# Kernel tuning notes

Hardware: AMD Instinct MI355X
Metric: run time of the kernel (lower is better)

## Reference

```python
import jax, jax.numpy as jnp
import numpy as np

B, N, U, D = 64, 1024, 128, 2   # batch, num_nodes, num_units, output_dim
K, L = 2, 2                     # max_diffusion_step, num_layers
NM = 2 * K + 1                  # num_matrices: 2 supports (dual random walk) * K + identity


def setup_inputs():
    key = jax.random.key(0)
    ks = jax.random.split(key, 16)
    d0, d1 = D + U, U + U       # gconv input_size per layer
    s = 0.05
    return {
        "inputs": jax.random.normal(ks[0], (B, N * D), jnp.float32),
        "hidden_state": jax.random.normal(ks[1], (L, B, N * U), jnp.float32),
        "adj": jax.random.uniform(ks[2], (N, N), dtype=jnp.float32),
        "gate_w0": jax.random.normal(ks[3], (d0 * NM, 2 * U), jnp.float32) * s,
        "gate_b0": jnp.ones((2 * U,), jnp.float32),   # bias_start=1.0 as in DCGRU gate
        "cand_w0": jax.random.normal(ks[4], (d0 * NM, U), jnp.float32) * s,
        "cand_b0": jnp.zeros((U,), jnp.float32),
        "gate_w1": jax.random.normal(ks[5], (d1 * NM, 2 * U), jnp.float32) * s,
        "gate_b1": jnp.ones((2 * U,), jnp.float32),
        "cand_w1": jax.random.normal(ks[6], (d1 * NM, U), jnp.float32) * s,
        "cand_b1": jnp.zeros((U,), jnp.float32),
        "proj_w": jax.random.normal(ks[7], (U, D), jnp.float32) * s,
        "proj_b": jnp.zeros((D,), jnp.float32),
    }


def _supports(adj):
    # dual random walk: [ (D_o^-1 A)^T, (D_i^-1 A^T)^T ]
    rw = lambda a: a / jnp.sum(a, axis=1, keepdims=True)
    return [rw(adj).T, rw(adj.T).T]


def _gconv(supports, x_bnd, h_bnd, w, b):
    # x_bnd: (B,N,in_dim), h_bnd: (B,N,U)
    in_size = x_bnd.shape[-1] + U
    x0 = jnp.transpose(jnp.concatenate([x_bnd, h_bnd], axis=-1), (1, 2, 0)).reshape(N, in_size * B)
    xs = [x0]
    for S in supports:
        xk_2, xk_1 = x0, S @ x0
        xs.append(xk_1)
        for _ in range(2, K + 1):
            xk = 2.0 * (S @ xk_1) - xk_2   # Chebyshev recursion
            xs.append(xk)
            xk_2, xk_1 = xk_1, xk
    x = jnp.stack(xs)                                   # (NM, N, in_size*B)
    x = x.reshape(NM, N, in_size, B).transpose(3, 1, 2, 0).reshape(B * N, in_size * NM)
    return x @ w + b                                    # (B*N, out)


def _dcgru_cell(supports, x_flat, h_flat, gw, gb, cw, cb, in_dim):
    xb = x_flat.reshape(B, N, in_dim)
    hb = h_flat.reshape(B, N, U)
    ru = jax.nn.sigmoid(_gconv(supports, xb, hb, gw, gb)).reshape(B, N, 2 * U)
    r, u = ru[..., :U], ru[..., U:]
    c = jnp.tanh(_gconv(supports, xb, r * hb, cw, cb)).reshape(B, N, U)
    return (u * hb + (1.0 - u) * c).reshape(B, N * U)


def reference(inputs, hidden_state, adj, gate_w0, gate_b0, cand_w0, cand_b0,
              gate_w1, gate_b1, cand_w1, cand_b1, proj_w, proj_b):
    sup = _supports(adj)
    h0 = _dcgru_cell(sup, inputs, hidden_state[0], gate_w0, gate_b0, cand_w0, cand_b0, D)
    h1 = _dcgru_cell(sup, h0, hidden_state[1], gate_w1, gate_b1, cand_w1, cand_b1, U)
    out = (h1.reshape(B * N, U) @ proj_w + proj_b).reshape(B, N * D)
    return out, jnp.stack([h0, h1])
```

## Files before the change

kernel.cpp:

```cpp
#include <hip/hip_runtime.h>
#include <hip/hip_bf16.h>

typedef unsigned short u16;
typedef unsigned int u32;
typedef __attribute__((ext_vector_type(2))) unsigned int u32x2;
typedef __attribute__((ext_vector_type(4))) float f32x4;
typedef __attribute__((ext_vector_type(8))) __bf16 bf16x8;

#define DEVI static __device__ __forceinline__

DEVI u16 f2bf(float x) {
  union { float f; u32 u; } v; v.f = x;
  u32 r = v.u + 0x7fffu + ((v.u >> 16) & 1u);
  return (u16)(r >> 16);
}
DEVI float bf2f(u16 h) { union { u32 u; float f; } v; v.u = ((u32)h) << 16; return v.f; }
DEVI u32 pk2bf(float a, float b) { return (u32)f2bf(a) | ((u32)f2bf(b) << 16); }
DEVI float sigm(float x) { return 1.f / (1.f + __expf(-x)); }
DEVI float tanh_(float x) {
  float a = fabsf(x);
  float e = __expf(-2.f * a);
  float t = (1.f - e) / (1.f + e);
  return copysignf(t, x);
}

DEVI void gl_lds16(const u16* g, void* l) {
  __builtin_amdgcn_global_load_lds(
      (const __attribute__((address_space(1))) u32*)(const void*)g,
      (__attribute__((address_space(3))) u32*)l, 16, 0, 0);
}
DEVI f32x4 mfma16(bf16x8 a, bf16x8 b, f32x4 c) {
  return __builtin_amdgcn_mfma_f32_16x16x32_bf16(a, b, c, 0, 0, 0);
}

#define SWZ(row) (((row) >> 1) & 3)

__global__ void sums_k(const float* __restrict__ adj, float* __restrict__ rs, float* __restrict__ cs) {
  __shared__ float red[256];
  int bid = blockIdx.x, tid = threadIdx.x;
  if (bid < 1024) {
    float a = 0.f;
    for (int j = tid; j < 1024; j += 256) a += adj[bid * 1024 + j];
    red[tid] = a; __syncthreads();
    for (int s = 128; s; s >>= 1) { if (tid < s) red[tid] += red[tid + s]; __syncthreads(); }
    if (!tid) rs[bid] = red[0];
  } else {
    int c0 = (bid - 1024) * 64;
    int c = tid & 63, r0 = tid >> 6;
    float a = 0.f;
    for (int r = r0; r < 1024; r += 4) a += adj[r * 1024 + c0 + c];
    red[tid] = a; __syncthreads();
    if (tid < 64) cs[c0 + c] = red[c] + red[64 + c] + red[128 + c] + red[192 + c];
  }
}

__global__ void s0_build(const float* __restrict__ adj, const float* __restrict__ rs, u16* __restrict__ S0) {
  __shared__ float tile[32][33];
  int i0 = blockIdx.x * 32, j0 = blockIdx.y * 32;
  int tx = threadIdx.x & 31, ty = threadIdx.x >> 5;
  for (int yy = ty; yy < 32; yy += 8)
    tile[yy][tx] = adj[(j0 + yy) * 1024 + i0 + tx];
  __syncthreads();
  for (int yy = ty; yy < 32; yy += 8)
    S0[(i0 + yy) * 1024 + j0 + tx] = f2bf(tile[tx][yy] / rs[j0 + tx]);
}

__global__ void s1_build(const float* __restrict__ adj, const float* __restrict__ cs, u16* __restrict__ S1) {
  int idx = blockIdx.x * 256 + threadIdx.x;
  int j = idx & 1023;
  S1[idx] = f2bf(adj[idx] / cs[j]);
}

__global__ void pack_w(const float* __restrict__ src, u16* __restrict__ dst,
                       int NO, int Ktot, int off0, int off1) {
  int idx = blockIdx.x * 256 + threadIdx.x;
  if (idx >= NO * Ktot) return;
  int o = idx / Ktot, k = idx % Ktot;
  int seg = k >> 7, i = k & 127;
  int mo = seg % 5;
  int pos = ((seg / 5) ? off1 : off0) + i;
  const float* wr = src + (long)pos * 5 * NO + o;
  float v;
  switch (mo) {
    case 0: v = wr[0] - wr[(long)2 * NO] - wr[(long)4 * NO]; break;
    case 1: v = wr[(long)1 * NO]; break;
    case 2: v = 2.f * wr[(long)2 * NO]; break;
    case 3: v = wr[(long)3 * NO]; break;
    default: v = 2.f * wr[(long)4 * NO]; break;
  }
  dst[idx] = f2bf(v);
}

__global__ void build_hx(const float* __restrict__ src, u16* __restrict__ hiN,
                         u16* __restrict__ hiT) {
  __shared__ u16 t[32][33];
  int n0 = blockIdx.x * 32, u0 = blockIdx.y * 32, b = blockIdx.z;
  int tx = threadIdx.x & 31, ty = threadIdx.x >> 5;
  for (int yy = ty; yy < 32; yy += 8) {
    long d = (long)b * 131072 + (n0 + yy) * 128 + u0 + tx;
    u16 h = f2bf(src[d]);
    hiN[d] = h;
    t[yy][tx] = h;
  }
  __syncthreads();
  for (int yy = ty; yy < 32; yy += 8)
    hiT[(long)(b * 128 + u0 + yy) * 1024 + n0 + tx] = t[tx][yy];
}

__global__ void xch0_build(const float* __restrict__ inp, float* __restrict__ x0) {
  int idx = blockIdx.x * 256 + threadIdx.x;
  int n = idx >> 7, c = idx & 127, b = c >> 1, d = c & 1;
  x0[idx] = inp[b * 2048 + n * 2 + d];
}

struct XJob { const u16* S; const float* xin; const float* x0; float* xout; };
struct XJobs { XJob j[2]; };
__global__ void xch_step2(XJobs js) {
  XJob J = js.j[blockIdx.z];
  int n = blockIdx.x, c = threadIdx.x;
  float acc = 0.f;
  for (int k = 0; k < 1024; k++) acc += bf2f(J.S[n * 1024 + k]) * J.xin[k * 128 + c];
  J.xout[n * 128 + c] = (J.x0 != nullptr) ? (2.f * acc - J.x0[n * 128 + c]) : acc;
}

__global__ __launch_bounds__(256) void xg_build(
    const float* __restrict__ gw0, const float* __restrict__ cw0,
    const float* __restrict__ xch,
    u16* __restrict__ xgg, u16* __restrict__ xgc) {
  __shared__ float wg[10][256];
  __shared__ float wc[10][128];
  __shared__ float xv[10];
  int t = threadIdx.x;
#pragma unroll
  for (int q = 0; q < 10; q++) {
    int m = q % 5, p = q / 5;
    wg[q][t] = gw0[(long)(p * 5 + m) * 256 + t];
    if (t < 128) wc[q][t] = cw0[(long)(p * 5 + m) * 128 + t];
  }
  __syncthreads();
  int r0 = blockIdx.x * 32;
  for (int rl = 0; rl < 32; rl++) {
    int r = r0 + rl, n = r & 1023, b = r >> 10;
    if (t < 10) { int m = t % 5, p = t / 5; xv[t] = xch[(long)m * 131072 + n * 128 + b * 2 + p]; }
    __syncthreads();
    float a = 0.f;
#pragma unroll
    for (int q = 0; q < 10; q++) a += wg[q][t] * xv[q];
    xgg[(long)r * 256 + t] = f2bf(a);
    if (t < 128) {
      float a2 = 0.f;
#pragma unroll
      for (int q = 0; q < 10; q++) a2 += wc[q][t] * xv[q];
      xgc[(long)r * 128 + t] = f2bf(a2);
    }
    __syncthreads();
  }
}

struct DiffJob { const u16* X; const u16* S; u16* YN; u16* YT; };
struct DiffJobs { DiffJob j[4]; };

__global__ __launch_bounds__(256, 2) void gemm_diffz(DiffJobs jobs) {
  DiffJob J = jobs.j[blockIdx.z];
  constexpr int BUF = 384 * 64;
  __shared__ char smem[3 * BUF];
  const int tid = threadIdx.x, wid = tid >> 6, lane = tid & 63;
  const int wrM = wid >> 1, wcN = wid & 1, l15 = lane & 15, l4 = lane >> 4;
  const int s_row = lane >> 2, s_kcp = lane & 3;
  const int l = blockIdx.y * 64 + blockIdx.x;
  const int sl = (l & 7) * 32 + (l >> 3);
  const int fbase = (sl >> 2) * 128;
  const int ntile = (sl & 3) * 256;

  f32x4 acc[8][4];
#pragma unroll
  for (int i = 0; i < 8; i++)
#pragma unroll
    for (int j = 0; j < 4; j++) acc[i][j] = (f32x4){0.f, 0.f, 0.f, 0.f};

  auto stage = [&](char* buf, int ks) {
    const int k0 = ks * 32;
#pragma unroll
    for (int c = 0; c < 6; c++) {
      const int row0 = c * 64 + wid * 16;
      const int row = row0 + s_row;
      const u16* src;
      if (row0 < 256) src = J.S + (long)(ntile + row) * 1024 + k0 + ((s_kcp ^ SWZ(row)) * 8);
      else { const int fr = row - 256; src = J.X + (long)(fbase + fr) * 1024 + k0 + ((s_kcp ^ SWZ(fr)) * 8); }
      gl_lds16(src, buf + row0 * 64);
    }
  };
  auto compute = [&](char* buf) {
    char* Ab = buf; char* Bb = buf + 256 * 64;
    bf16x8 af[8], bfr[4];
#pragma unroll
    for (int mb = 0; mb < 8; mb++) {
      const int row = wrM * 128 + mb * 16 + l15;
      af[mb] = *(const bf16x8*)(Ab + row * 64 + ((l4 ^ SWZ(row)) * 16));
    }
#pragma unroll
    for (int nb = 0; nb < 4; nb++) {
      const int row = wcN * 64 + nb * 16 + l15;
      bfr[nb] = *(const bf16x8*)(Bb + row * 64 + ((l4 ^ SWZ(row)) * 16));
    }
    __builtin_amdgcn_s_setprio(1);
#pragma unroll
    for (int mb = 0; mb < 8; mb++)
#pragma unroll
      for (int nb = 0; nb < 4; nb++)
        acc[mb][nb] = mfma16(af[mb], bfr[nb], acc[mb][nb]);
    __builtin_amdgcn_s_setprio(0);
  };

  const int NKS = 32;
  stage(smem, 0);
  stage(smem + BUF, 1);
  char* cur = smem; char* mid = smem + BUF; char* fut = smem + 2 * BUF;
  for (int ks = 0; ks + 2 < NKS; ks++) {
    stage(fut, ks + 2);
    asm volatile("s_waitcnt vmcnt(12)" ::: "memory");
    __builtin_amdgcn_s_barrier();
    __builtin_amdgcn_sched_barrier(0);
    compute(cur);
    asm volatile("" ::: "memory");
    __builtin_amdgcn_s_barrier();
    __builtin_amdgcn_sched_barrier(0);
    char* t = cur; cur = mid; mid = fut; fut = t;
  }
  asm volatile("s_waitcnt vmcnt(6)" ::: "memory");
  __builtin_amdgcn_s_barrier();
  __builtin_amdgcn_sched_barrier(0);
  compute(cur);
  asm volatile("s_waitcnt vmcnt(0)" ::: "memory");
  __builtin_amdgcn_s_barrier();
  __builtin_amdgcn_sched_barrier(0);
  compute(mid);

#pragma unroll
  for (int mb = 0; mb < 8; mb++) {
#pragma unroll
    for (int nb = 0; nb < 4; nb++) {
      const int n0 = ntile + wrM * 128 + mb * 16 + l4 * 4;
      const int f  = fbase + wcN * 64 + nb * 16 + l15;
      const int b = f >> 7, u = f & 127;
      f32x4 v = acc[mb][nb];
      u16 h0 = f2bf(v[0]), h1 = f2bf(v[1]), h2 = f2bf(v[2]), h3 = f2bf(v[3]);
      u16* yn = J.YN + (long)b * 131072 + (long)n0 * 128 + u;
      yn[0] = h0; yn[128] = h1; yn[256] = h2; yn[384] = h3;
      if (J.YT != nullptr) {
        u32x2 wv; wv[0] = (u32)h0 | ((u32)h1 << 16); wv[1] = (u32)h2 | ((u32)h3 << 16);
        *(u32x2*)(J.YT + (long)f * 1024 + n0) = wv;
      }
    }
  }
}

struct Segs { const u16* p[10]; };
DEVI const u16* seg_sel(const Segs& s, int i) {
  switch (i) {
    case 0: return s.p[0]; case 1: return s.p[1]; case 2: return s.p[2];
    case 3: return s.p[3]; case 4: return s.p[4]; case 5: return s.p[5];
    case 6: return s.p[6]; case 7: return s.p[7]; case 8: return s.p[8];
    default: return s.p[9];
  }
}

template<int EPI>
__global__ __launch_bounds__(256, 2) void gemm_wseg(
    Segs segs, const u16* __restrict__ WT, int Ktot,
    const float* __restrict__ bias, const float* __restrict__ Hprev,
    const u16* __restrict__ Hb16,
    const u16* __restrict__ xadd,
    u16* __restrict__ rh_hi, u16* __restrict__ rh_t, u16* __restrict__ usig,
    float* __restrict__ hnew_out, u16* __restrict__ xa_hi, u16* __restrict__ xa_t)
{
  constexpr int TM = (EPI == 0) ? 256 : 128;
  constexpr int MB = (EPI == 0) ? 8 : 4;
  constexpr int MW = (EPI == 0) ? 128 : 64;
  constexpr int R1 = (TM + 128) / 64;
  constexpr int BUF = (TM + 128) * 64;
  __shared__ char smem[3 * BUF];
  const int tid = threadIdx.x, wid = tid >> 6, lane = tid & 63;
  const int wrM = wid >> 1, wcN = wid & 1, l15 = lane & 15, l4 = lane >> 4;
  const int s_row = lane >> 2, s_kcp = lane & 3;
  const int rtile = blockIdx.x * 128;

  f32x4 acc[MB][4];
#pragma unroll
  for (int i = 0; i < MB; i++)
#pragma unroll
    for (int j = 0; j < 4; j++) acc[i][j] = (f32x4){0.f, 0.f, 0.f, 0.f};

  const int NKS = Ktot >> 5;
  auto stage = [&](char* buf, int ks) {
    const int k0 = ks * 32;
    const int sidx = ks >> 2, si0 = (ks & 3) * 32;
    const u16* sp = seg_sel(segs, sidx);
#pragma unroll
    for (int c = 0; c < R1; c++) {
      const int row0 = c * 64 + wid * 16;
      const int row = row0 + s_row;
      const u16* src;
      if (row0 < TM) src = WT + (long)row * Ktot + k0 + ((s_kcp ^ SWZ(row)) * 8);
      else { const int br = row - TM; src = sp + (long)(rtile + br) * 128 + si0 + ((s_kcp ^ SWZ(br)) * 8); }
      gl_lds16(src, buf + row0 * 64);
    }
  };
  auto compute = [&](char* buf) {
    char* Ab = buf; char* Bb = buf + TM * 64;
    bf16x8 af[MB], bfr[4];
#pragma unroll
    for (int mb = 0; mb < MB; mb++) {
      const int row = wrM * MW + mb * 16 + l15;
      af[mb] = *(const bf16x8*)(Ab + row * 64 + ((l4 ^ SWZ(row)) * 16));
    }
#pragma unroll
    for (int nb = 0; nb < 4; nb++) {
      const int row = wcN * 64 + nb * 16 + l15;
      bfr[nb] = *(const bf16x8*)(Bb + row * 64 + ((l4 ^ SWZ(row)) * 16));
    }
    __builtin_amdgcn_s_setprio(1);
#pragma unroll
    for (int mb = 0; mb < MB; mb++)
#pragma unroll
      for (int nb = 0; nb < 4; nb++)
        acc[mb][nb] = mfma16(af[mb], bfr[nb], acc[mb][nb]);
    __builtin_amdgcn_s_setprio(0);
  };

  stage(smem, 0);
  stage(smem + BUF, 1);
  char* cur = smem; char* mid = smem + BUF; char* fut = smem + 2 * BUF;
  for (int ks = 0; ks + 2 < NKS; ks++) {
    stage(fut, ks + 2);
    if constexpr (R1 == 6) asm volatile("s_waitcnt vmcnt(12)" ::: "memory");
    else                   asm volatile("s_waitcnt vmcnt(8)" ::: "memory");
    __builtin_amdgcn_s_barrier();
    __builtin_amdgcn_sched_barrier(0);
    compute(cur);
    asm volatile("" ::: "memory");
    __builtin_amdgcn_s_barrier();
    __builtin_amdgcn_sched_barrier(0);
    char* t = cur; cur = mid; mid = fut; fut = t;
  }
  if constexpr (R1 == 6) asm volatile("s_waitcnt vmcnt(6)" ::: "memory");
  else                   asm volatile("s_waitcnt vmcnt(4)" ::: "memory");
  __builtin_amdgcn_s_barrier();
  __builtin_amdgcn_sched_barrier(0);
  compute(cur);
  asm volatile("s_waitcnt vmcnt(0)" ::: "memory");
  __builtin_amdgcn_s_barrier();
  __builtin_amdgcn_sched_barrier(0);
  compute(mid);

#pragma unroll
  for (int mb = 0; mb < MB; mb++) {
#pragma unroll
    for (int nb = 0; nb < 4; nb++) {
      const int o = wrM * MW + mb * 16 + l4 * 4;
      const int rr = rtile + wcN * 64 + nb * 16 + l15;
      const int n = rr & 1023, b = rr >> 10;
      f32x4 v = acc[mb][nb];
      float4 bv = *(const float4*)(bias + o);
      float a0 = 0.f, a1 = 0.f, a2 = 0.f, a3 = 0.f;
      if (xadd != nullptr) {
        const int xs = (EPI == 0) ? 256 : 128;
        u32x2 xv = *(const u32x2*)(xadd + (long)rr * xs + o);
        a0 = bf2f((u16)(xv[0] & 0xffffu)); a1 = bf2f((u16)(xv[0] >> 16));
        a2 = bf2f((u16)(xv[1] & 0xffffu)); a3 = bf2f((u16)(xv[1] >> 16));
      }
      float hx0, hx1, hx2, hx3;
      if (Hb16 != nullptr) {
        u32x2 hv2 = *(const u32x2*)(Hb16 + (long)rr * 128 + o);
        hx0 = bf2f((u16)(hv2[0] & 0xffffu)); hx1 = bf2f((u16)(hv2[0] >> 16));
        hx2 = bf2f((u16)(hv2[1] & 0xffffu)); hx3 = bf2f((u16)(hv2[1] >> 16));
      } else {
        float4 hv = *(const float4*)(Hprev + (long)rr * 128 + o);
        hx0 = hv.x; hx1 = hv.y; hx2 = hv.z; hx3 = hv.w;
      }
      if (EPI == 0) {
        float s0 = sigm(v[0] + bv.x + a0), s1 = sigm(v[1] + bv.y + a1);
        float s2 = sigm(v[2] + bv.z + a2), s3 = sigm(v[3] + bv.w + a3);
        if (o < 128) {
          float r0 = s0 * hx0, r1 = s1 * hx1, r2 = s2 * hx2, r3 = s3 * hx3;
          u16 h0 = f2bf(r0), h1 = f2bf(r1), h2 = f2bf(r2), h3 = f2bf(r3);
          long d = (long)rr * 128 + o;
          u32x2 wh; wh[0] = (u32)h0 | ((u32)h1 << 16); wh[1] = (u32)h2 | ((u32)h3 << 16);
          *(u32x2*)(rh_hi + d) = wh;
          u16* rt = rh_t + (long)(b * 128 + o) * 1024 + n;
          rt[0] = h0; rt[1024] = h1; rt[2048] = h2; rt[3072] = h3;
        } else {
          u32x2 wu; wu[0] = pk2bf(s0, s1); wu[1] = pk2bf(s2, s3);
          *(u32x2*)(usig + (long)rr * 128 + (o - 128)) = wu;
        }
      } else {
        float c0 = tanh_(v[0] + bv.x + a0), c1 = tanh_(v[1] + bv.y + a1);
        float c2 = tanh_(v[2] + bv.z + a2), c3 = tanh_(v[3] + bv.w + a3);
        u32x2 uv = *(const u32x2*)(usig + (long)rr * 128 + o);
        float u0 = bf2f((u16)(uv[0] & 0xffffu)), u1 = bf2f((u16)(uv[0] >> 16));
        float u2 = bf2f((u16)(uv[1] & 0xffffu)), u3 = bf2f((u16)(uv[1] >> 16));
        float h0n = u0 * hx0 + (1.f - u0) * c0;
        float h1n = u1 * hx1 + (1.f - u1) * c1;
        float h2n = u2 * hx2 + (1.f - u2) * c2;
        float h3n = u3 * hx3 + (1.f - u3) * c3;
        *(float4*)(hnew_out + (long)rr * 128 + o) = make_float4(h0n, h1n, h2n, h3n);
        if (xa_hi != nullptr) {
          u16 x0 = f2bf(h0n), x1 = f2bf(h1n), x2 = f2bf(h2n), x3 = f2bf(h3n);
          long d = (long)rr * 128 + o;
          u32x2 wh; wh[0] = (u32)x0 | ((u32)x1 << 16); wh[1] = (u32)x2 | ((u32)x3 << 16);
          *(u32x2*)(xa_hi + d) = wh;
          u16* xt = xa_t + (long)(b * 128 + o) * 1024 + n;
          xt[0] = x0; xt[1024] = x1; xt[2048] = x2; xt[3072] = x3;
        }
      }
    }
  }
}

__global__ __launch_bounds__(256) void proj_k(const float* __restrict__ h1n, const float* __restrict__ pw,
                                              const float* __restrict__ pb, float* __restrict__ out) {
  int wid = threadIdx.x >> 6, lane = threadIdx.x & 63;
  int r = blockIdx.x * 4 + wid;
  int b = r >> 10, n = r & 1023;
  const float* hp = h1n + (long)b * 131072 + n * 128;
  float ha = hp[lane], hb = hp[lane + 64];
  float p0 = ha * pw[lane * 2]     + hb * pw[(lane + 64) * 2];
  float p1 = ha * pw[lane * 2 + 1] + hb * pw[(lane + 64) * 2 + 1];
  for (int off = 32; off; off >>= 1) { p0 += __shfl_down(p0, off); p1 += __shfl_down(p1, off); }
  if (!lane) {
    out[(long)b * 2048 + n * 2]     = p0 + pb[0];
    out[(long)b * 2048 + n * 2 + 1] = p1 + pb[1];
  }
}

extern "C" void kernel_launch(void* const* d_in, const int* in_sizes, int n_in,
                              void* d_out, int out_size, void* d_ws, size_t ws_size,
                              hipStream_t stream) {
  (void)in_sizes; (void)n_in; (void)out_size; (void)ws_size;
  const float* inputs = (const float*)d_in[0];
  const float* hidden = (const float*)d_in[1];
  const float* adj    = (const float*)d_in[2];
  const float* gw0 = (const float*)d_in[3];
  const float* gb0 = (const float*)d_in[4];
  const float* cw0 = (const float*)d_in[5];
  const float* cb0 = (const float*)d_in[6];
  const float* gw1 = (const float*)d_in[7];
  const float* gb1 = (const float*)d_in[8];
  const float* cw1 = (const float*)d_in[9];
  const float* cb1 = (const float*)d_in[10];
  const float* pw  = (const float*)d_in[11];
  const float* pb  = (const float*)d_in[12];

  float* out    = (float*)d_out;
  float* out_h0 = out + 131072;
  float* out_h1 = out_h0 + 8388608;
  const float* h0 = hidden;
  const float* h1 = hidden + 8388608;

  u16* OH1a = (u16*)out_h1;

  char* wp = (char*)d_ws;
  auto alloc = [&](size_t bytes) { char* r = wp; wp += (bytes + 255) & ~(size_t)255; return r; };
  u16*   S0b  = (u16*)  alloc(1048576 * 2);
  u16*   S1b  = (u16*)  alloc(1048576 * 2);
  float* rs   = (float*)alloc(1024 * 4);
  float* cs   = (float*)alloc(1024 * 4);
  u16*   WG0  = (u16*)  alloc((size_t)256 * 640 * 2);
  u16*   WC0  = (u16*)  alloc((size_t)128 * 640 * 2);
  u16*   WG1  = (u16*)  alloc((size_t)256 * 1280 * 2);
  u16*   WC1  = (u16*)  alloc((size_t)128 * 1280 * 2);
  u16*   Bb   = (u16*)  alloc((size_t)13 * 8388608 * 2);
  u16*   USIG = (u16*)  alloc((size_t)8388608 * 2);
  float* XCH  = (float*)alloc((size_t)5 * 131072 * 4);
  auto BB = [&](int i) { return Bb + (size_t)i * 8388608; };
  auto XC = [&](int i) { return XCH + (size_t)i * 131072; };
  u16* XGg = BB(3);
  u16* XGc = BB(5);

  sums_k<<<1040, 256, 0, stream>>>(adj, rs, cs);
  s0_build<<<dim3(32, 32), 256, 0, stream>>>(adj, rs, S0b);
  s1_build<<<4096, 256, 0, stream>>>(adj, cs, S1b);
  pack_w<<<640,  256, 0, stream>>>(gw0, WG0, 256, 640, 2, 0);
  pack_w<<<320,  256, 0, stream>>>(cw0, WC0, 128, 640, 2, 0);
  pack_w<<<1280, 256, 0, stream>>>(gw1, WG1, 256, 1280, 0, 128);
  pack_w<<<640,  256, 0, stream>>>(cw1, WC1, 128, 1280, 0, 128);
  build_hx<<<dim3(32, 4, 64), 256, 0, stream>>>(h0, BB(0), BB(1));
  build_hx<<<dim3(32, 4, 64), 256, 0, stream>>>(h1, OH1a, BB(2));

  xch0_build<<<512, 256, 0, stream>>>(inputs, XC(0));
  XJobs xj{};
  xj.j[0] = {S0b, XC(0), nullptr, XC(1)};
  xj.j[1] = {S1b, XC(0), nullptr, XC(3)};
  xch_step2<<<dim3(1024, 1, 2), 128, 0, stream>>>(xj);
  xj.j[0] = {S0b, XC(1), XC(0), XC(2)};
  xj.j[1] = {S1b, XC(3), XC(0), XC(4)};
  xch_step2<<<dim3(1024, 1, 2), 128, 0, stream>>>(xj);
  xg_build<<<2048, 256, 0, stream>>>(gw0, cw0, XCH, XGg, XGc);

  DiffJobs dj{};
  dj.j[0] = {BB(1), S0b, BB(6), BB(7)};
  dj.j[1] = {BB(1), S1b, BB(8), BB(9)};
  gemm_diffz<<<dim3(64, 4, 2), 256, 0, stream>>>(dj);
  dj.j[0] = {BB(7), S0b, BB(10), nullptr};
  dj.j[1] = {BB(9), S1b, BB(11), nullptr};
  gemm_diffz<<<dim3(64, 4, 2), 256, 0, stream>>>(dj);

  Segs sg0{};
  sg0.p[0] = BB(0); sg0.p[1] = BB(6); sg0.p[2] = BB(10); sg0.p[3] = BB(8); sg0.p[4] = BB(11);
  gemm_wseg<0><<<512, 256, 0, stream>>>(sg0, WG0, 640, gb0, h0, BB(0), XGg,
      BB(12), BB(1), USIG, nullptr, nullptr, nullptr);

  dj.j[0] = {BB(1), S0b, BB(6), BB(7)};
  dj.j[1] = {BB(1), S1b, BB(8), BB(9)};
  gemm_diffz<<<dim3(64, 4, 2), 256, 0, stream>>>(dj);
  dj.j[0] = {BB(7), S0b, BB(10), nullptr};
  dj.j[1] = {BB(9), S1b, BB(11), nullptr};
  gemm_diffz<<<dim3(64, 4, 2), 256, 0, stream>>>(dj);

  Segs sc0{};
  sc0.p[0] = BB(12); sc0.p[1] = BB(6); sc0.p[2] = BB(10); sc0.p[3] = BB(8); sc0.p[4] = BB(11);
  gemm_wseg<1><<<512, 256, 0, stream>>>(sc0, WC0, 640, cb0, h0, BB(0), XGc,
      nullptr, nullptr, USIG, out_h0, BB(0), BB(1));

  dj.j[0] = {BB(1), S0b, BB(3), BB(4)};
  dj.j[1] = {BB(1), S1b, BB(5), BB(6)};
  dj.j[2] = {BB(2), S0b, BB(7), BB(8)};
  dj.j[3] = {BB(2), S1b, BB(9), BB(10)};
  gemm_diffz<<<dim3(64, 4, 4), 256, 0, stream>>>(dj);
  dj.j[0] = {BB(4), S0b, BB(11), nullptr};
  dj.j[1] = {BB(6), S1b, BB(12), nullptr};
  gemm_diffz<<<dim3(64, 4, 2), 256, 0, stream>>>(dj);
  dj.j[0] = {BB(8), S0b, BB(4), nullptr};
  dj.j[1] = {BB(10), S1b, BB(6), nullptr};
  gemm_diffz<<<dim3(64, 4, 2), 256, 0, stream>>>(dj);

  Segs sg1{};
  sg1.p[0] = BB(0); sg1.p[1] = BB(3); sg1.p[2] = BB(11); sg1.p[3] = BB(5); sg1.p[4] = BB(12);
  sg1.p[5] = OH1a;  sg1.p[6] = BB(7); sg1.p[7] = BB(4);  sg1.p[8] = BB(9); sg1.p[9] = BB(6);
  gemm_wseg<0><<<512, 256, 0, stream>>>(sg1, WG1, 1280, gb1, h1, OH1a, nullptr,
      BB(8), BB(10), USIG, nullptr, nullptr, nullptr);

  dj.j[0] = {BB(10), S0b, BB(1), BB(2)};
  dj.j[1] = {BB(10), S1b, BB(7), BB(9)};
  gemm_diffz<<<dim3(64, 4, 2), 256, 0, stream>>>(dj);
  dj.j[0] = {BB(2), S0b, BB(4), nullptr};
  dj.j[1] = {BB(9), S1b, BB(6), nullptr};
  gemm_diffz<<<dim3(64, 4, 2), 256, 0, stream>>>(dj);

  Segs sc1{};
  sc1.p[0] = BB(0); sc1.p[1] = BB(3); sc1.p[2] = BB(11); sc1.p[3] = BB(5); sc1.p[4] = BB(12);
  sc1.p[5] = BB(8); sc1.p[6] = BB(1); sc1.p[7] = BB(4);  sc1.p[8] = BB(7); sc1.p[9] = BB(6);
  gemm_wseg<1><<<512, 256, 0, stream>>>(sc1, WC1, 1280, cb1, h1, nullptr, nullptr,
      nullptr, nullptr, USIG, out_h1, nullptr, nullptr);

  proj_k<<<16384, 256, 0, stream>>>(out_h1, pw, pb, out);
}
```

Measured before the change: 961.5 us.

## Precompute squared supports so each diffusion stage is one batched GEMM launch

Computes S0·S0 and S1·S1 once with the diffusion GEMM, using new transposed support copies and a new epilogue that writes a square result. Every later two-step Chebyshev diffusion (S·x then S·(S·x)) then runs as four independent GEMMs against X in a single launch instead of two dependent launches. This removes a serial dependency and the transposed intermediate writes, and doubles the parallel work per launch. The cost is an extra 1024³ GEMM per support up front, more workspace, and a different bf16 rounding path, since S² is rounded before it multiplies X.

```diff
diff --git a/kernel.cpp b/kernel.cpp
--- a/kernel.cpp
+++ b/kernel.cpp
@@ -54,21 +54,32 @@
   }
 }
 
-__global__ void s0_build(const float* __restrict__ adj, const float* __restrict__ rs, u16* __restrict__ S0) {
+__global__ void s0t_build(const float* __restrict__ adj, const float* __restrict__ rs,
+                          u16* __restrict__ S0, u16* __restrict__ S0T) {
   __shared__ float tile[32][33];
   int i0 = blockIdx.x * 32, j0 = blockIdx.y * 32;
   int tx = threadIdx.x & 31, ty = threadIdx.x >> 5;
   for (int yy = ty; yy < 32; yy += 8)
     tile[yy][tx] = adj[(j0 + yy) * 1024 + i0 + tx];
   __syncthreads();
+  for (int yy = ty; yy < 32; yy += 8) {
+    S0 [(i0 + yy) * 1024 + j0 + tx] = f2bf(tile[tx][yy] / rs[j0 + tx]);
+    S0T[(j0 + yy) * 1024 + i0 + tx] = f2bf(tile[yy][tx] / rs[j0 + yy]);
+  }
+}
+
+__global__ void s1t_build(const float* __restrict__ adj, const float* __restrict__ cs,
+                          u16* __restrict__ S1, u16* __restrict__ S1T) {
+  __shared__ float tile[32][33];
+  int i0 = blockIdx.x * 32, j0 = blockIdx.y * 32;
+  int tx = threadIdx.x & 31, ty = threadIdx.x >> 5;
   for (int yy = ty; yy < 32; yy += 8)
-    S0[(i0 + yy) * 1024 + j0 + tx] = f2bf(tile[tx][yy] / rs[j0 + tx]);
-}
-
-__global__ void s1_build(const float* __restrict__ adj, const float* __restrict__ cs, u16* __restrict__ S1) {
-  int idx = blockIdx.x * 256 + threadIdx.x;
-  int j = idx & 1023;
-  S1[idx] = f2bf(adj[idx] / cs[j]);
+    tile[yy][tx] = adj[(i0 + yy) * 1024 + j0 + tx];
+  __syncthreads();
+  for (int yy = ty; yy < 32; yy += 8) {
+    S1 [(i0 + yy) * 1024 + j0 + tx] = f2bf(tile[yy][tx] / cs[j0 + tx]);
+    S1T[(j0 + yy) * 1024 + i0 + tx] = f2bf(tile[tx][yy] / cs[j0 + yy]);
+  }
 }
 
 __global__ void pack_w(const float* __restrict__ src, u16* __restrict__ dst,
@@ -157,7 +168,7 @@
   }
 }
 
-struct DiffJob { const u16* X; const u16* S; u16* YN; u16* YT; };
+struct DiffJob { const u16* X; const u16* S; u16* YN; u16* YS; };
 struct DiffJobs { DiffJob j[4]; };
 
 __global__ __launch_bounds__(256, 2) void gemm_diffz(DiffJobs jobs) {
@@ -167,10 +178,16 @@
   const int tid = threadIdx.x, wid = tid >> 6, lane = tid & 63;
   const int wrM = wid >> 1, wcN = wid & 1, l15 = lane & 15, l4 = lane >> 4;
   const int s_row = lane >> 2, s_kcp = lane & 3;
-  const int l = blockIdx.y * 64 + blockIdx.x;
-  const int sl = (l & 7) * 32 + (l >> 3);
-  const int fbase = (sl >> 2) * 128;
-  const int ntile = (sl & 3) * 256;
+  int fbase, ntile;
+  if (gridDim.x == 64) {
+    const int l = blockIdx.y * 64 + blockIdx.x;
+    const int sl = (l & 7) * 32 + (l >> 3);
+    fbase = (sl >> 2) * 128;
+    ntile = (sl & 3) * 256;
+  } else {
+    fbase = blockIdx.x * 128;
+    ntile = blockIdx.y * 256;
+  }
 
   f32x4 acc[8][4];
 #pragma unroll
@@ -242,14 +259,15 @@
     for (int nb = 0; nb < 4; nb++) {
       const int n0 = ntile + wrM * 128 + mb * 16 + l4 * 4;
       const int f  = fbase + wcN * 64 + nb * 16 + l15;
-      const int b = f >> 7, u = f & 127;
       f32x4 v = acc[mb][nb];
       u16 h0 = f2bf(v[0]), h1 = f2bf(v[1]), h2 = f2bf(v[2]), h3 = f2bf(v[3]);
-      u16* yn = J.YN + (long)b * 131072 + (long)n0 * 128 + u;
-      yn[0] = h0; yn[128] = h1; yn[256] = h2; yn[384] = h3;
-      if (J.YT != nullptr) {
-        u32x2 wv; wv[0] = (u32)h0 | ((u32)h1 << 16); wv[1] = (u32)h2 | ((u32)h3 << 16);
-        *(u32x2*)(J.YT + (long)f * 1024 + n0) = wv;
+      if (J.YN != nullptr) {
+        const int b = f >> 7, u = f & 127;
+        u16* yn = J.YN + (long)b * 131072 + (long)n0 * 128 + u;
+        yn[0] = h0; yn[128] = h1; yn[256] = h2; yn[384] = h3;
+      } else {
+        u16* ys = J.YS + (long)n0 * 1024 + f;
+        ys[0] = h0; ys[1024] = h1; ys[2048] = h2; ys[3072] = h3;
       }
     }
   }
@@ -463,6 +481,10 @@
   auto alloc = [&](size_t bytes) { char* r = wp; wp += (bytes + 255) & ~(size_t)255; return r; };
   u16*   S0b  = (u16*)  alloc(1048576 * 2);
   u16*   S1b  = (u16*)  alloc(1048576 * 2);
+  u16*   S0Tb = (u16*)  alloc(1048576 * 2);
+  u16*   S1Tb = (u16*)  alloc(1048576 * 2);
+  u16*   SQ0  = (u16*)  alloc(1048576 * 2);
+  u16*   SQ1  = (u16*)  alloc(1048576 * 2);
   float* rs   = (float*)alloc(1024 * 4);
   float* cs   = (float*)alloc(1024 * 4);
   u16*   WG0  = (u16*)  alloc((size_t)256 * 640 * 2);
@@ -478,14 +500,19 @@
   u16* XGc = BB(5);
 
   sums_k<<<1040, 256, 0, stream>>>(adj, rs, cs);
-  s0_build<<<dim3(32, 32), 256, 0, stream>>>(adj, rs, S0b);
-  s1_build<<<4096, 256, 0, stream>>>(adj, cs, S1b);
+  s0t_build<<<dim3(32, 32), 256, 0, stream>>>(adj, rs, S0b, S0Tb);
+  s1t_build<<<dim3(32, 32), 256, 0, stream>>>(adj, cs, S1b, S1Tb);
   pack_w<<<640,  256, 0, stream>>>(gw0, WG0, 256, 640, 2, 0);
   pack_w<<<320,  256, 0, stream>>>(cw0, WC0, 128, 640, 2, 0);
   pack_w<<<1280, 256, 0, stream>>>(gw1, WG1, 256, 1280, 0, 128);
   pack_w<<<640,  256, 0, stream>>>(cw1, WC1, 128, 1280, 0, 128);
   build_hx<<<dim3(32, 4, 64), 256, 0, stream>>>(h0, BB(0), BB(1));
   build_hx<<<dim3(32, 4, 64), 256, 0, stream>>>(h1, OH1a, BB(2));
+
+  DiffJobs dj{};
+  dj.j[0] = {S0Tb, S0b, nullptr, SQ0};
+  dj.j[1] = {S1Tb, S1b, nullptr, SQ1};
+  gemm_diffz<<<dim3(8, 4, 2), 256, 0, stream>>>(dj);
 
   xch0_build<<<512, 256, 0, stream>>>(inputs, XC(0));
   XJobs xj{};
@@ -497,59 +524,54 @@
   xch_step2<<<dim3(1024, 1, 2), 128, 0, stream>>>(xj);
   xg_build<<<2048, 256, 0, stream>>>(gw0, cw0, XCH, XGg, XGc);
 
-  DiffJobs dj{};
-  dj.j[0] = {BB(1), S0b, BB(6), BB(7)};
-  dj.j[1] = {BB(1), S1b, BB(8), BB(9)};
-  gemm_diffz<<<dim3(64, 4, 2), 256, 0, stream>>>(dj);
-  dj.j[0] = {BB(7), S0b, BB(10), nullptr};
-  dj.j[1] = {BB(9), S1b, BB(11), nullptr};
-  gemm_diffz<<<dim3(64, 4, 2), 256, 0, stream>>>(dj);
+  dj.j[0] = {BB(1), S0b, BB(6), nullptr};
+  dj.j[1] = {BB(1), SQ0, BB(7), nullptr};
+  dj.j[2] = {BB(1), S1b, BB(8), nullptr};
+  dj.j[3] = {BB(1), SQ1, BB(9), nullptr};
+  gemm_diffz<<<dim3(64, 4, 4), 256, 0, stream>>>(dj);
 
   Segs sg0{};
-  sg0.p[0] = BB(0); sg0.p[1] = BB(6); sg0.p[2] = BB(10); sg0.p[3] = BB(8); sg0.p[4] = BB(11);
+  sg0.p[0] = BB(0); sg0.p[1] = BB(6); sg0.p[2] = BB(7); sg0.p[3] = BB(8); sg0.p[4] = BB(9);
   gemm_wseg<0><<<512, 256, 0, stream>>>(sg0, WG0, 640, gb0, h0, BB(0), XGg,
-      BB(12), BB(1), USIG, nullptr, nullptr, nullptr);
-
-  dj.j[0] = {BB(1), S0b, BB(6), BB(7)};
-  dj.j[1] = {BB(1), S1b, BB(8), BB(9)};
-  gemm_diffz<<<dim3(64, 4, 2), 256, 0, stream>>>(dj);
-  dj.j[0] = {BB(7), S0b, BB(10), nullptr};
-  dj.j[1] = {BB(9), S1b, BB(11), nullptr};
-  gemm_diffz<<<dim3(64, 4, 2), 256, 0, stream>>>(dj);
+      BB(10), BB(11), USIG, nullptr, nullptr, nullptr);
+
+  dj.j[0] = {BB(11), S0b, BB(6), nullptr};
+  dj.j[1] = {BB(11), SQ0, BB(7), nullptr};
+  dj.j[2] = {BB(11), S1b, BB(8), nullptr};
+  dj.j[3] = {BB(11), SQ1, BB(9), nullptr};
+  gemm_diffz<<<dim3(64, 4, 4), 256, 0, stream>>>(dj);
 
   Segs sc0{};
-  sc0.p[0] = BB(12); sc0.p[1] = BB(6); sc0.p[2] = BB(10); sc0.p[3] = BB(8); sc0.p[4] = BB(11);
+  sc0.p[0] = BB(10); sc0.p[1] = BB(6); sc0.p[2] = BB(7); sc0.p[3] = BB(8); sc0.p[4] = BB(9);
   gemm_wseg<1><<<512, 256, 0, stream>>>(sc0, WC0, 640, cb0, h0, BB(0), XGc,
       nullptr, nullptr, USIG, out_h0, BB(0), BB(1));
 
-  dj.j[0] = {BB(1), S0b, BB(3), BB(4)};
-  dj.j[1] = {BB(1), S1b, BB(5), BB(6)};
-  dj.j[2] = {BB(2), S0b, BB(7), BB(8)};
-  dj.j[3] = {BB(2), S1b, BB(9), BB(10)};
+  dj.j[0] = {BB(1), S0b, BB(3), nullptr};
+  dj.j[1] = {BB(1), SQ0, BB(4), nullptr};
+  dj.j[2] = {BB(1), S1b, BB(5), nullptr};
+  dj.j[3] = {BB(1), SQ1, BB(6), nullptr};
   gemm_diffz<<<dim3(64, 4, 4), 256, 0, stream>>>(dj);
-  dj.j[0] = {BB(4), S0b, BB(11), nullptr};
-  dj.j[1] = {BB(6), S1b, BB(12), nullptr};
-  gemm_diffz<<<dim3(64, 4, 2), 256, 0, stream>>>(dj);
-  dj.j[0] = {BB(8), S0b, BB(4), nullptr};
-  dj.j[1] = {BB(10), S1b, BB(6), nullptr};
-  gemm_diffz<<<dim3(64, 4, 2), 256, 0, stream>>>(dj);
+  dj.j[0] = {BB(2), S0b, BB(7), nullptr};
+  dj.j[1] = {BB(2), SQ0, BB(8), nullptr};
+  dj.j[2] = {BB(2), S1b, BB(9), nullptr};
+  dj.j[3] = {BB(2), SQ1, BB(10), nullptr};
+  gemm_diffz<<<dim3(64, 4, 4), 256, 0, stream>>>(dj);
 
   Segs sg1{};
-  sg1.p[0] = BB(0); sg1.p[1] = BB(3); sg1.p[2] = BB(11); sg1.p[3] = BB(5); sg1.p[4] = BB(12);
-  sg1.p[5] = OH1a;  sg1.p[6] = BB(7); sg1.p[7] = BB(4);  sg1.p[8] = BB(9); sg1.p[9] = BB(6);
+  sg1.p[0] = BB(0); sg1.p[1] = BB(3); sg1.p[2] = BB(4); sg1.p[3] = BB(5); sg1.p[4] = BB(6);
+  sg1.p[5] = OH1a;  sg1.p[6] = BB(7); sg1.p[7] = BB(8); sg1.p[8] = BB(9); sg1.p[9] = BB(10);
   gemm_wseg<0><<<512, 256, 0, stream>>>(sg1, WG1, 1280, gb1, h1, OH1a, nullptr,
-      BB(8), BB(10), USIG, nullptr, nullptr, nullptr);
-
-  dj.j[0] = {BB(10), S0b, BB(1), BB(2)};
-  dj.j[1] = {BB(10), S1b, BB(7), BB(9)};
-  gemm_diffz<<<dim3(64, 4, 2), 256, 0, stream>>>(dj);
-  dj.j[0] = {BB(2), S0b, BB(4), nullptr};
-  dj.j[1] = {BB(9), S1b, BB(6), nullptr};
-  gemm_diffz<<<dim3(64, 4, 2), 256, 0, stream>>>(dj);
+      BB(11), BB(12), USIG, nullptr, nullptr, nullptr);
+
+  dj.j[0] = {BB(12), S0b, BB(1), nullptr};
+  dj.j[1] = {BB(12), SQ0, BB(2), nullptr};
+  dj.j[2] = {BB(12), S1b, BB(7), nullptr};
+  dj.j[3] = {BB(12), SQ1, BB(8), nullptr};
+  gemm_diffz<<<dim3(64, 4, 4), 256, 0, stream>>>(dj);
 
   Segs sc1{};
-  sc1.p[0] = BB(0); sc1.p[1] = BB(3); sc1.p[2] = BB(11); sc1.p[3] = BB(5); sc1.p[4] = BB(12);
-  sc1.p[5] = BB(8); sc1.p[6] = BB(1); sc1.p[7] = BB(4);  sc1.p[8] = BB(7); sc1.p[9] = BB(6);
+  sc1.p[0] = BB(0);  sc1.p[1] = BB(3); sc1.p[2] = BB(4); sc1.p[3] = BB(5); sc1.p[4] = BB(6);
+  sc1.p[5] = BB(11); sc1.p[6] = BB(1); sc1.p[7] = BB(2); sc1.p[8] = BB(7); sc1.p[9] = BB(8);
   gemm_wseg<1><<<512, 256, 0, stream>>>(sc1, WC1, 1280, cb1, h1, nullptr, nullptr,
       nullptr, nullptr, USIG, out_h1, nullptr, nullptr);
 
```

New measurement: 922.1 us. 4.1% less time.
